# Optimization experiments

Hardware: AMD Instinct MI355X
Metric: run time of the kernel (lower is better)

## Reference

```python
import jax, jax.numpy as jnp
import numpy as np

B, LENGTH = 4, 65494
FILTS = 256        # sinc out channels == attention seq len == d_model (BN constraint)
KERNEL = 1025      # first_conv=1024 -> forced odd
D_MODEL = 256
N_HEADS = 8
D_FF = 1024
E_LAYERS = 4
C_OUT = 2
IN_SIZE = 21490
SR = 16000


def _to_mel(hz):
    return 2595 * np.log10(1 + hz / 700)


def _to_hz(mel):
    return 700 * (10 ** (mel / 2595) - 1)


def make_sinc_filters():
    out_ch = FILTS + 1
    f = (SR // 2) * np.linspace(0, 1, 257)  # NFFT=512 -> 257 bins
    fmel = _to_mel(f)
    mels = np.linspace(fmel.min(), fmel.max(), out_ch + 2)
    freq = _to_hz(mels)[:out_ch]
    hsupp = np.arange(-(KERNEL - 1) / 2, (KERNEL - 1) / 2 + 1)
    ham = np.hamming(KERNEL)
    bp = np.zeros((FILTS, KERNEL), dtype=np.float32)
    for i in range(FILTS):
        fmin, fmax = freq[i], freq[i + 1]
        h_hi = 2 * fmax / SR * np.sinc(2 * fmax * hsupp / SR)
        h_lo = 2 * fmin / SR * np.sinc(2 * fmin * hsupp / SR)
        bp[i] = (ham * (h_hi - h_lo)).astype(np.float32)
    return jnp.asarray(bp).reshape(FILTS, 1, KERNEL)


def layernorm(x, g, b, eps=1e-5):
    m = x.mean(-1, keepdims=True)
    v = x.var(-1, keepdims=True)
    return (x - m) / jnp.sqrt(v + eps) * g + b


def batchnorm(x, g, b, eps=1e-5):
    # training-mode BatchNorm1d over [B, C, T]: stats over (0, 2)
    m = x.mean((0, 2), keepdims=True)
    v = x.var((0, 2), keepdims=True)
    return (x - m) / jnp.sqrt(v + eps) * g[None, :, None] + b[None, :, None]


def positional(n):
    pos = jnp.arange(n, dtype=jnp.float32)[:, None]
    div = jnp.exp(jnp.arange(0, D_MODEL, 2, dtype=jnp.float32) * (-np.log(10000.0) / D_MODEL))
    pe = jnp.zeros((n, D_MODEL), jnp.float32)
    pe = pe.at[:, 0::2].set(jnp.sin(pos * div)).at[:, 1::2].set(jnp.cos(pos * div))
    return pe


def _forward(x, filters, bn1_g, bn1_b, emb_w, emb_b, embbn_g, embbn_b,
             wq, bq, wk, bk, wv, bv, wo, bo, c1w, c1b, c2w, c2b,
             ln1g, ln1b, ln2g, ln2b, lnfg, lnfb, projw, projb):
    Bb = x.shape[0]
    # SincConv: [B,1,L] -> [B, FILTS, L-K+1]
    h = jax.lax.conv_general_dilated(x[:, None, :], filters, (1,), 'VALID',
                                     dimension_numbers=('NCH', 'OIH', 'NCH'))
    h = jnp.abs(h)
    T = h.shape[-1] // 3
    h = h[..., :T * 3].reshape(Bb, FILTS, T, 3).max(-1)  # max_pool1d(k=3)
    h = jax.nn.selu(batchnorm(h, bn1_g, bn1_b))          # [B, FILTS, 21490]
    # LinearEmbedding: Linear(21490 -> d_model) + BN + ReLU + pos emb
    e = jnp.einsum('bct,dt->bcd', h, emb_w) + emb_b      # [B, FILTS, D_MODEL]
    e = jax.nn.relu(batchnorm(e, embbn_g, embbn_b))
    z = e + positional(e.shape[1])[None]
    hd = D_MODEL // N_HEADS
    scale = 1.0 / np.sqrt(hd)
    for l in range(E_LAYERS):
        q = (z @ wq[l].T + bq[l]).reshape(Bb, FILTS, N_HEADS, hd)
        k = (z @ wk[l].T + bk[l]).reshape(Bb, FILTS, N_HEADS, hd)
        v = (z @ wv[l].T + bv[l]).reshape(Bb, FILTS, N_HEADS, hd)
        scores = jnp.einsum('blhe,bshe->bhls', q, k) * scale  # mask_flag=False
        attn = jax.nn.softmax(scores, axis=-1)
        o = jnp.einsum('bhls,bshd->blhd', attn, v).reshape(Bb, FILTS, D_MODEL)
        o = o @ wo[l].T + bo[l]
        z = layernorm(z + o, ln1g[l], ln1b[l])
        y = jax.nn.gelu(jnp.einsum('bld,fd->blf', z, c1w[l]) + c1b[l], approximate=False)
        y = jnp.einsum('blf,df->bld', y, c2w[l]) + c2b[l]
        z = layernorm(z + y, ln2g[l], ln2b[l])
    z = layernorm(z, lnfg, lnfb)
    pooled = z.mean(axis=1)
    return pooled @ projw.T + projb  # [B, C_OUT]


def setup_inputs() -> dict:
    key = jax.random.key(0)
    ks = jax.random.split(key, 16)
    rn = lambda k, s, sc=0.02: jax.random.normal(k, s, jnp.float32) * sc
    d = {}
    d['x'] = jax.random.normal(ks[0], (B, LENGTH), jnp.float32)
    d['filters'] = make_sinc_filters()
    d['bn1_g'] = jnp.ones((FILTS,), jnp.float32)
    d['bn1_b'] = jnp.zeros((FILTS,), jnp.float32)
    d['emb_w'] = rn(ks[1], (D_MODEL, IN_SIZE))
    d['emb_b'] = jnp.zeros((D_MODEL,), jnp.float32)
    d['embbn_g'] = jnp.ones((D_MODEL,), jnp.float32)
    d['embbn_b'] = jnp.zeros((D_MODEL,), jnp.float32)
    d['wq'] = rn(ks[2], (E_LAYERS, D_MODEL, D_MODEL))
    d['bq'] = jnp.zeros((E_LAYERS, D_MODEL), jnp.float32)
    d['wk'] = rn(ks[3], (E_LAYERS, D_MODEL, D_MODEL))
    d['bk'] = jnp.zeros((E_LAYERS, D_MODEL), jnp.float32)
    d['wv'] = rn(ks[4], (E_LAYERS, D_MODEL, D_MODEL))
    d['bv'] = jnp.zeros((E_LAYERS, D_MODEL), jnp.float32)
    d['wo'] = rn(ks[5], (E_LAYERS, D_MODEL, D_MODEL))
    d['bo'] = jnp.zeros((E_LAYERS, D_MODEL), jnp.float32)
    d['c1w'] = rn(ks[6], (E_LAYERS, D_FF, D_MODEL))
    d['c1b'] = jnp.zeros((E_LAYERS, D_FF), jnp.float32)
    d['c2w'] = rn(ks[7], (E_LAYERS, D_MODEL, D_FF))
    d['c2b'] = jnp.zeros((E_LAYERS, D_MODEL), jnp.float32)
    d['ln1g'] = jnp.ones((E_LAYERS, D_MODEL), jnp.float32)
    d['ln1b'] = jnp.zeros((E_LAYERS, D_MODEL), jnp.float32)
    d['ln2g'] = jnp.ones((E_LAYERS, D_MODEL), jnp.float32)
    d['ln2b'] = jnp.zeros((E_LAYERS, D_MODEL), jnp.float32)
    d['lnfg'] = jnp.ones((D_MODEL,), jnp.float32)
    d['lnfb'] = jnp.zeros((D_MODEL,), jnp.float32)
    d['projw'] = rn(ks[8], (C_OUT, D_MODEL))
    d['projb'] = jnp.zeros((C_OUT,), jnp.float32)
    return d


def reference(x, filters, bn1_g, bn1_b, emb_w, emb_b, embbn_g, embbn_b,
              wq, bq, wk, bk, wv, bv, wo, bo, c1w, c1b, c2w, c2b,
              ln1g, ln1b, ln2g, ln2b, lnfg, lnfb, projw, projb):
    return _forward(x, filters, bn1_g, bn1_b, emb_w, emb_b, embbn_g, embbn_b,
                    wq, bq, wk, bk, wv, bv, wo, bo, c1w, c1b, c2w, c2b,
                    ln1g, ln1b, ln2g, ln2b, lnfg, lnfb, projw, projb)
```

## Files before the change

kernel.cpp:

```cpp
#include <hip/hip_runtime.h>
#include <math.h>

#define L_IN 65494
#define T_POOL 21490
#define TPP 21496
#define KF 1025
#define RS 1144
#define NCH 141
#define KEMB 21490
#define KEMBP 21504
#define NKC 1344
#define FTILE 33280
#define LWSZ 786432

typedef short s16x4 __attribute__((ext_vector_type(4)));
typedef _Float16 f16x8 __attribute__((ext_vector_type(8)));
typedef float f32x4 __attribute__((ext_vector_type(4)));
typedef float f32x16 __attribute__((ext_vector_type(16)));

__device__ inline float selu_f(float x) {
    float e = expf(fminf(x, 0.f));
    float neg = 1.6732632423543772f * (e - 1.f);
    return 1.0507009873554805f * (x > 0.f ? x : neg);
}

__device__ inline float gelu_f(float x) {
    return 0.5f * x * (1.f + erff(x * 0.7071067811865476f));
}

__device__ inline float dot4(float4 a, float4 b) {
    return fmaf(a.x, b.x, fmaf(a.y, b.y, fmaf(a.z, b.z, a.w * b.w)));
}

__device__ inline float sel4(float a0, float a1, float a2, float a3, int i) {
    float r = a0;
    r = (i == 1) ? a1 : r;
    r = (i == 2) ? a2 : r;
    r = (i == 3) ? a3 : r;
    return r;
}

__device__ inline short f2h_bits(float v) {
    _Float16 h = (_Float16)v;
    return *(short*)&h;
}

__device__ inline void f16split2(float v, _Float16& h, _Float16& l) {
    h = (_Float16)v;
    l = (_Float16)(v - (float)h);
}

__global__ __launch_bounds__(512)
void pack_all_kernel(const float* __restrict__ filt, const float* __restrict__ emb_w,
                     const float* __restrict__ wo, const float* __restrict__ wq,
                     const float* __restrict__ wk, const float* __restrict__ wv,
                     const float* __restrict__ c1w, const float* __restrict__ c2w,
                     short* __restrict__ fpH, short* __restrict__ wpH,
                     short* __restrict__ lw) {
    int bx = blockIdx.x;
    int t = threadIdx.x, lane = t >> 3, e = t & 7;
    if (bx < 520) {
        int ft = bx / 65, kc = bx % 65;
        int f = ft * 32 + (lane & 31);
        int tap = kc * 16 + (lane >> 5) * 8 + e;
        float v = (tap < KF) ? filt[f * KF + tap] : 0.f;
        fpH[bx * 512 + t] = f2h_bits(v);
    } else if (bx < 520 + 8 * NKC) {
        int blk = bx - 520;
        int ft = blk / NKC, kc = blk % NKC;
        int row = ft * 32 + (lane & 31);
        int tap = kc * 16 + (lane >> 5) * 8 + e;
        float v = (tap < KEMB) ? emb_w[(long)row * KEMB + tap] : 0.f;
        wpH[(long)blk * 512 + t] = f2h_bits(v);
    } else {
        int b = bx - 520 - 8 * NKC;
        int layer = b / 1536, r = b % 1536;
        const float* src;
        int K, t2;
        long dst;
        if (r < 512) {
            int mat = r >> 7; t2 = r & 127;
            const float* m0 = (mat == 0 ? wo : mat == 1 ? wq : mat == 2 ? wk : wv);
            src = m0 + (long)layer * 65536; K = 256;
            dst = (long)layer * LWSZ + (long)mat * 65536 + (long)t2 * 512;
        } else if (r < 1024) {
            t2 = r - 512;
            src = c1w + (long)layer * 262144; K = 256;
            dst = (long)layer * LWSZ + 262144 + (long)t2 * 512;
        } else {
            t2 = r - 1024;
            src = c2w + (long)layer * 262144; K = 1024;
            dst = (long)layer * LWSZ + 524288 + (long)t2 * 512;
        }
        int KB = K >> 5;
        int nt = t2 / KB, kb = t2 % KB;
        int n = nt * 16 + (lane & 15);
        int k = kb * 32 + ((lane >> 4) & 3) * 8 + e;
        lw[dst + t] = f2h_bits(src[(long)n * K + k]);
    }
}

__device__ inline f32x4 mfma_nt(const _Float16* __restrict__ Xh, const _Float16* __restrict__ Xl,
                                int xstride, const short* __restrict__ wp_nt, int KB, int lane) {
    f32x4 acc = {0.f, 0.f, 0.f, 0.f};
    const int row = (lane & 15) & 3;
    const int ko0 = ((lane >> 4) & 3) * 8;
    const short* bp = wp_nt + lane * 8;
    const _Float16* xh = Xh + row * xstride + ko0;
    const _Float16* xl = Xl + row * xstride + ko0;
#pragma unroll 8
    for (int kb = 0; kb < KB; kb++) {
        f16x8 bf = *(const f16x8*)(bp + kb * 512);
        f16x8 ah = *(const f16x8*)(xh + kb * 32);
        f16x8 al = *(const f16x8*)(xl + kb * 32);
        acc = __builtin_amdgcn_mfma_f32_16x16x32_f16(al, bf, acc, 0, 0, 0);
        acc = __builtin_amdgcn_mfma_f32_16x16x32_f16(ah, bf, acc, 0, 0, 0);
    }
    return acc;
}

union ConvLDS {
    short xh[8][RS];
    float ebuf[96][129];
};

__global__ __launch_bounds__(256, 3)
void conv_mfma_kernel(const float* __restrict__ x, const short* __restrict__ fpH,
                      _Float16* __restrict__ h) {
    __shared__ ConvLDS u;
    const int tid = threadIdx.x;
    const int pb = blockIdx.x;
    const int b = blockIdx.y;
    const int t0 = pb * 96;
    const float* xb = x + (long)b * L_IN;

    if (pb < 671) {
        for (int idx = tid; idx < 8 * NCH; idx += 256) {
            int s = idx / NCH, j = idx - s * NCH;
            int gi = t0 + s + j * 8;
            f16x8 hv;
#pragma unroll
            for (int e = 0; e < 8; e++) hv[e] = (_Float16)xb[gi + e];
            *(f16x8*)&u.xh[s][j * 8] = hv;
        }
    } else {
        for (int idx = tid; idx < 8 * NCH; idx += 256) {
            int s = idx / NCH, j = idx - s * NCH;
            int gi = t0 + s + j * 8;
            f16x8 hv;
#pragma unroll
            for (int e = 0; e < 8; e++) {
                float v = (gi + e < L_IN) ? xb[gi + e] : 0.f;
                hv[e] = (_Float16)v;
            }
            *(f16x8*)&u.xh[s][j * 8] = hv;
        }
    }
    __syncthreads();

    const int lane = tid & 63;
    const int wid = tid >> 6;
    const int l31 = lane & 31;
    const int hi = lane >> 5;
    const int f0w = wid * 64;

    const short* aH = &u.xh[l31 & 7][8 * (l31 >> 3) + 8 * hi];
    const short* bp0 = fpH + (long)(wid * 2) * FTILE + lane * 8;
    const short* bp1 = bp0 + FTILE;

    f32x16 a00 = {0}, a01 = {0}, a10 = {0}, a11 = {0}, a20 = {0}, a21 = {0};

#pragma unroll 1
    for (int kc = 0; kc < 65; kc++) {
        const int ko = kc * 16;
        const int kf = kc * 512;
        f16x8 ah0 = *(const f16x8*)(aH + ko);
        f16x8 ah1 = *(const f16x8*)(aH + ko + 32);
        f16x8 ah2 = *(const f16x8*)(aH + ko + 64);
        f16x8 bh0 = *(const f16x8*)(bp0 + kf);
        f16x8 bh1 = *(const f16x8*)(bp1 + kf);
        a00 = __builtin_amdgcn_mfma_f32_32x32x16_f16(ah0, bh0, a00, 0, 0, 0);
        a01 = __builtin_amdgcn_mfma_f32_32x32x16_f16(ah0, bh1, a01, 0, 0, 0);
        a10 = __builtin_amdgcn_mfma_f32_32x32x16_f16(ah1, bh0, a10, 0, 0, 0);
        a11 = __builtin_amdgcn_mfma_f32_32x32x16_f16(ah1, bh1, a11, 0, 0, 0);
        a20 = __builtin_amdgcn_mfma_f32_32x32x16_f16(ah2, bh0, a20, 0, 0, 0);
        a21 = __builtin_amdgcn_mfma_f32_32x32x16_f16(ah2, bh1, a21, 0, 0, 0);
    }

    __syncthreads();
    const int t3l = tid & 31;
    const int t3 = pb * 32 + t3l;

#pragma unroll
    for (int half = 0; half < 2; half++) {
        if ((wid >> 1) == half) {
            int fcb = f0w - half * 128;
#define WRF(ACC, MT, NT)                                                   \
            {                                                              \
                int fc = fcb + NT * 32 + l31;                              \
                _Pragma("unroll")                                          \
                for (int r = 0; r < 16; r++) {                             \
                    int pos = MT * 32 + (r & 3) + 8 * (r >> 2) + 4 * hi;   \
                    u.ebuf[pos][fc] = fabsf(ACC[r]);                       \
                }                                                          \
            }
            WRF(a00, 0, 0) WRF(a01, 0, 1)
            WRF(a10, 1, 0) WRF(a11, 1, 1)
            WRF(a20, 2, 0) WRF(a21, 2, 1)
#undef WRF
        }
        __syncthreads();
        if (t3 < T_POOL) {
            for (int ff = tid >> 5; ff < 128; ff += 8) {
                float v = fmaxf(fmaxf(u.ebuf[3 * t3l][ff], u.ebuf[3 * t3l + 1][ff]),
                                u.ebuf[3 * t3l + 2][ff]);
                h[((long)(b * 256 + half * 128 + ff)) * TPP + t3] = (_Float16)v;
            }
        }
        __syncthreads();
    }
}

__global__ __launch_bounds__(256)
void bn_part_kernel(const _Float16* __restrict__ xin, float* __restrict__ p1,
                    float* __restrict__ p2) {
    __shared__ float sm[8];
    int c = blockIdx.x, s = blockIdx.y, tid = threadIdx.x;
    int t0 = s * 2687, t1 = min(T_POOL, t0 + 2687);
    float s1 = 0.f, s2 = 0.f;
    for (int b = 0; b < 4; b++) {
        const _Float16* p = xin + (long)b * 256 * TPP + (long)c * TPP;
        for (int t = t0 + tid; t < t1; t += 256) {
            float v = (float)p[t];
            s1 += v;
            s2 = fmaf(v, v, s2);
        }
    }
    for (int off = 32; off > 0; off >>= 1) { s1 += __shfl_down(s1, off); s2 += __shfl_down(s2, off); }
    int lane = tid & 63, wv = tid >> 6;
    if (lane == 0) { sm[wv] = s1; sm[4 + wv] = s2; }
    __syncthreads();
    if (tid == 0) {
        p1[c * 8 + s] = sm[0] + sm[1] + sm[2] + sm[3];
        p2[c * 8 + s] = sm[4] + sm[5] + sm[6] + sm[7];
    }
}

__global__ __launch_bounds__(256)
void bn_fin_kernel(const float* __restrict__ p1, const float* __restrict__ p2,
                   const float* __restrict__ g, const float* __restrict__ bb,
                   float* __restrict__ sc, float* __restrict__ sh) {
    int c = threadIdx.x;
    float S1 = 0.f, S2 = 0.f;
#pragma unroll
    for (int s = 0; s < 8; s++) { S1 += p1[c * 8 + s]; S2 += p2[c * 8 + s]; }
    float n = 4.f * (float)T_POOL;
    float mean = S1 / n;
    float var = S2 / n - mean * mean;
    float rstd = rsqrtf(var + 1e-5f);
    float gc = g[c], bc = bb[c];
    sc[c] = rstd * gc;
    sh[c] = bc - mean * rstd * gc;
}

__global__ __launch_bounds__(256, 2)
void embed_mfma_kernel(const _Float16* __restrict__ H, const short* __restrict__ Wh,
                       const float* __restrict__ sc, const float* __restrict__ sh,
                       float* __restrict__ P, int kPerZ) {
    __shared__ short Ah[128][36];
    const int tid = threadIdx.x;
    const int rowBase = blockIdx.x * 128;
    const int colBase = blockIdx.y * 128;
    const int z = blockIdx.z;
    const int kz = z * kPerZ;
    const int iters = kPerZ >> 5;

    const int trow = tid >> 1, th = (tid & 1) * 16;
    const int arow = rowBase + trow;
    const float asc = sc[arow & 255], ash_ = sh[arow & 255];
    const _Float16* Ap = H + (long)arow * TPP;

    const int lane = tid & 63, wid = tid >> 6;
    const int l31 = lane & 31, hi = lane >> 5;
    const int wm = wid >> 1, wn = wid & 1;

    const short* bhp[2];
#pragma unroll
    for (int nt = 0; nt < 2; nt++) {
        int ft = (colBase >> 5) + wn * 2 + nt;
        bhp[nt] = Wh + (long)ft * NKC * 512 + lane * 8;
    }

    f32x16 acc[2][2] = {{{0}, {0}}, {{0}, {0}}};

    for (int it = 0; it < iters; it++) {
        const int k0 = kz + it * 32;
        __syncthreads();
        float av[16];
        if (k0 + 32 <= KEMB) {
            const f16x8* p8 = (const f16x8*)(Ap + k0 + th);
            f16x8 v0 = p8[0], v1 = p8[1];
#pragma unroll
            for (int e = 0; e < 8; e++) { av[e] = (float)v0[e]; av[8 + e] = (float)v1[e]; }
        } else {
#pragma unroll
            for (int e = 0; e < 16; e++) {
                int k = k0 + th + e;
                av[e] = (k < KEMB) ? (float)Ap[k] : 0.f;
            }
        }
#pragma unroll
        for (int q = 0; q < 4; q++) {
            s16x4 h4;
#pragma unroll
            for (int e = 0; e < 4; e++) {
                float v = selu_f(fmaf(av[q * 4 + e], asc, ash_));
                h4[e] = f2h_bits(v);
            }
            *(s16x4*)&Ah[trow][th + q * 4] = h4;
        }
        __syncthreads();

#pragma unroll
        for (int ks = 0; ks < 2; ks++) {
            const int kloc = ks * 16 + hi * 8;
            const long kcg = (long)((k0 >> 4) + ks) * 512;
            f16x8 ah[2], bh[2];
#pragma unroll
            for (int mt = 0; mt < 2; mt++) {
                const int r = wm * 64 + mt * 32 + l31;
                const short* ph = &Ah[r][kloc];
                union { f16x8 v; unsigned long long q[2]; } uh;
                uh.q[0] = *(const unsigned long long*)(ph);
                uh.q[1] = *(const unsigned long long*)(ph + 4);
                ah[mt] = uh.v;
            }
#pragma unroll
            for (int nt = 0; nt < 2; nt++)
                bh[nt] = *(const f16x8*)(bhp[nt] + kcg);
#pragma unroll
            for (int mt = 0; mt < 2; mt++)
#pragma unroll
                for (int nt = 0; nt < 2; nt++)
                    acc[mt][nt] = __builtin_amdgcn_mfma_f32_32x32x16_f16(ah[mt], bh[nt], acc[mt][nt], 0, 0, 0);
        }
    }

    float* Pz = P + (long)z * 262144;
#pragma unroll
    for (int mt = 0; mt < 2; mt++)
#pragma unroll
        for (int nt = 0; nt < 2; nt++) {
            int col = colBase + wn * 64 + nt * 32 + l31;
#pragma unroll
            for (int r = 0; r < 16; r++) {
                int row = rowBase + wm * 64 + mt * 32 + (r & 3) + 8 * (r >> 2) + 4 * hi;
                Pz[(long)row * 256 + col] = acc[mt][nt][r];
            }
        }
}

__global__ __launch_bounds__(256)
void embed_combine_kernel(const float* __restrict__ P, const float* __restrict__ eb,
                          float* __restrict__ e, float* __restrict__ ebnp, int nsplit) {
    __shared__ float sm[8];
    const int bid = blockIdx.x, tid = threadIdx.x;
    const int idx = bid * 256 + tid;
    float s = 0.f;
    for (int z = 0; z < nsplit; z++) s += P[(long)z * 262144 + idx];
    float v = s + eb[tid];
    e[idx] = v;
    float s1 = v, s2 = v * v;
    for (int off = 32; off > 0; off >>= 1) { s1 += __shfl_down(s1, off); s2 += __shfl_down(s2, off); }
    int lane = tid & 63, wv = tid >> 6;
    if (lane == 0) { sm[wv] = s1; sm[4 + wv] = s2; }
    __syncthreads();
    if (tid == 0) {
        ebnp[bid * 2] = sm[0] + sm[1] + sm[2] + sm[3];
        ebnp[bid * 2 + 1] = sm[4] + sm[5] + sm[6] + sm[7];
    }
}

__global__ __launch_bounds__(512)
void qkv_init_kernel(const float* __restrict__ e, const float* __restrict__ ebnp,
                     const float* __restrict__ bng, const float* __restrict__ bnb,
                     const short* __restrict__ lw0,
                     const float* __restrict__ bq0, const float* __restrict__ bk0,
                     const float* __restrict__ bv0,
                     float* __restrict__ z, float* __restrict__ qo,
                     float* __restrict__ ko, float* __restrict__ vo) {
    __shared__ _Float16 zsh[4][256], zsl[4][256];
    __shared__ float scs[4], shs[4];
    const int t = threadIdx.x;
    const int w = t >> 6, lane = t & 63;
    const long rowg0 = (long)blockIdx.x * 4;

    if (t < 4) {
        int c = (int)((rowg0 + t) & 255);
        float S1 = 0.f, S2 = 0.f;
#pragma unroll
        for (int b2 = 0; b2 < 4; b2++) {
            S1 += ebnp[(b2 * 256 + c) * 2];
            S2 += ebnp[(b2 * 256 + c) * 2 + 1];
        }
        float mean = S1 * (1.f / 1024.f);
        float var = S2 * (1.f / 1024.f) - mean * mean;
        float rstd = rsqrtf(var + 1e-5f);
        float gc = bng[c];
        scs[t] = rstd * gc;
        shs[t] = bnb[c] - mean * rstd * gc;
    }
    __syncthreads();

    for (int idx = t; idx < 1024; idx += 512) {
        int i = idx >> 8, dd = idx & 255;
        int c = (int)((rowg0 + i) & 255);
        float v = fmaf(e[(rowg0 + i) * 256 + dd], scs[i], shs[i]);
        v = fmaxf(v, 0.f);
        int i2 = dd >> 1;
        float ang = (float)c * expf(-0.03597789207803195f * (float)(2 * i2));
        float pe = (dd & 1) ? cosf(ang) : sinf(ang);
        float zz = v + pe;
        z[(rowg0 + i) * 256 + dd] = zz;
        _Float16 hh, ll;
        f16split2(zz, hh, ll);
        zsh[i][dd] = hh; zsl[i][dd] = ll;
    }
    __syncthreads();

#pragma unroll
    for (int mat = 0; mat < 3; mat++) {
        const short* wp = lw0 + 65536 * (1 + mat);
        const float* bb = (mat == 0 ? bq0 : mat == 1 ? bk0 : bv0);
        float* op = (mat == 0 ? qo : mat == 1 ? ko : vo);
        for (int nt = w; nt < 16; nt += 8) {
            f32x4 acc = mfma_nt(&zsh[0][0], &zsl[0][0], 256, wp + nt * 8 * 512, 8, lane);
            if (lane < 16) {
                int col = nt * 16 + lane;
                float bv2 = bb[col];
#pragma unroll
                for (int r = 0; r < 4; r++)
                    op[(rowg0 + r) * 256 + col] = acc[r] + bv2;
            }
        }
    }
}

__device__ inline void ln_reduce4(const float (*buf)[256], float (*mr)[2], int t) {
    int wid = t >> 6, lane = t & 63;
    if (wid < 4) {
        float4 v = *(const float4*)&buf[wid][lane * 4];
        float s = v.x + v.y + v.z + v.w;
        float q = v.x * v.x + v.y * v.y + v.z * v.z + v.w * v.w;
#pragma unroll
        for (int off = 32; off > 0; off >>= 1) {
            s += __shfl_xor(s, off);
            q += __shfl_xor(q, off);
        }
        if (lane == 0) {
            float mean = s * (1.f / 256.f);
            float var = q * (1.f / 256.f) - mean * mean;
            mr[wid][0] = mean;
            mr[wid][1] = rsqrtf(var + 1e-5f);
        }
    }
}

template <int LAST>
__global__ __launch_bounds__(1024)
void layer_kernel(const float* __restrict__ zin, const float* __restrict__ qin,
                  const float* __restrict__ kin, const float* __restrict__ vin,
                  const short* __restrict__ lw_l, const short* __restrict__ lw_n,
                  const float* __restrict__ bo_l,
                  const float* __restrict__ c1b_l, const float* __restrict__ c2b_l,
                  const float* __restrict__ ln1g_l, const float* __restrict__ ln1b_l,
                  const float* __restrict__ ln2g_l, const float* __restrict__ ln2b_l,
                  const float* __restrict__ bq_n, const float* __restrict__ bk_n,
                  const float* __restrict__ bv_n,
                  const float* __restrict__ lnfg, const float* __restrict__ lnfb,
                  float* __restrict__ zout, float* __restrict__ qo,
                  float* __restrict__ ko, float* __restrict__ vo,
                  float* __restrict__ lnf_out) {
    __shared__ float zs[4][256];
    __shared__ float qb[4][256];
    __shared__ float sscore[4][8][256];
    __shared__ _Float16 zsh[4][256], zsl[4][256];
    __shared__ _Float16 yh[4][1024], yl[4][1024];
    __shared__ float mr[4][2];

    const int t = threadIdx.x;
    const int w = t >> 6, lane = t & 63;
    const long rowg0 = (long)blockIdx.x * 4;
    const int b = blockIdx.x >> 6;

    const int f = t & 255;
    const int kq = t >> 8;

    {
        int r = t >> 8, dd = t & 255;
        zs[r][dd] = zin[(rowg0 + r) * 256 + dd];
        qb[r][dd] = qin[(rowg0 + r) * 256 + dd];
    }
    __syncthreads();

    {
        const float scale = 0.17677669529663687f;
        const int jq = lane >> 3, li = lane & 7, d4 = li * 4;
        const int hh = w >> 1, jh = w & 1;
        const float* kb = kin + (long)b * 65536 + hh * 32 + d4;
        float4 q0 = *(const float4*)&qb[0][hh * 32 + d4];
        float4 q1 = *(const float4*)&qb[1][hh * 32 + d4];
        float4 q2 = *(const float4*)&qb[2][hh * 32 + d4];
        float4 q3 = *(const float4*)&qb[3][hh * 32 + d4];
        for (int jb = 0; jb < 16; jb++) {
            int j = jh * 128 + jb * 8 + jq;
            float4 kv = *(const float4*)(kb + (long)j * 256);
            float a0 = dot4(kv, q0), a1 = dot4(kv, q1);
            float a2 = dot4(kv, q2), a3 = dot4(kv, q3);
#pragma unroll
            for (int off = 1; off < 8; off <<= 1) {
                a0 += __shfl_xor(a0, off); a1 += __shfl_xor(a1, off);
                a2 += __shfl_xor(a2, off); a3 += __shfl_xor(a3, off);
            }
            if (li < 4) sscore[li][hh][j] = sel4(a0, a1, a2, a3, li) * scale;
        }
    }
    __syncthreads();

    {
#pragma unroll
        for (int p = 0; p < 2; p++) {
            int pair = w * 2 + p;
            int i = pair >> 3, hh = pair & 7;
            float* row = sscore[i][hh];
            float v0 = row[lane], v1 = row[lane + 64];
            float v2 = row[lane + 128], v3 = row[lane + 192];
            float m = fmaxf(fmaxf(v0, v1), fmaxf(v2, v3));
#pragma unroll
            for (int off = 32; off > 0; off >>= 1) m = fmaxf(m, __shfl_xor(m, off));
            float e0 = expf(v0 - m), e1 = expf(v1 - m);
            float e2 = expf(v2 - m), e3 = expf(v3 - m);
            float su = e0 + e1 + e2 + e3;
#pragma unroll
            for (int off = 32; off > 0; off >>= 1) su += __shfl_xor(su, off);
            float inv = 1.f / su;
            row[lane] = e0 * inv; row[lane + 64] = e1 * inv;
            row[lane + 128] = e2 * inv; row[lane + 192] = e3 * inv;
        }
    }
    __syncthreads();

    {
        int row = kq;
        int hh = f >> 5;
        const float* vcol = vin + (long)b * 65536 + f;
        const float* p0 = sscore[row][hh];
        float a0 = 0.f;
#pragma unroll 8
        for (int j4 = 0; j4 < 64; j4++) {
            float4 pv0 = *(const float4*)(p0 + j4 * 4);
            float v0 = vcol[(long)(j4 * 4 + 0) * 256];
            float v1 = vcol[(long)(j4 * 4 + 1) * 256];
            float v2 = vcol[(long)(j4 * 4 + 2) * 256];
            float v3 = vcol[(long)(j4 * 4 + 3) * 256];
            a0 = fmaf(pv0.x, v0, a0); a0 = fmaf(pv0.y, v1, a0);
            a0 = fmaf(pv0.z, v2, a0); a0 = fmaf(pv0.w, v3, a0);
        }
        _Float16 hh2, ll;
        f16split2(a0, hh2, ll);
        zsh[row][f] = hh2; zsl[row][f] = ll;
    }
    __syncthreads();

    {
        int nt = w;
        f32x4 acc = mfma_nt(&zsh[0][0], &zsl[0][0], 256, lw_l + nt * 8 * 512, 8, lane);
        if (lane < 16) {
            int col = nt * 16 + lane;
            float bb = bo_l[col];
#pragma unroll
            for (int r = 0; r < 4; r++)
                qb[r][col] = acc[r] + bb + zs[r][col];
        }
    }
    __syncthreads();
    ln_reduce4(qb, mr, t);
    __syncthreads();
    {
        int r = kq;
        float z1 = (qb[r][f] - mr[r][0]) * mr[r][1] * ln1g_l[f] + ln1b_l[f];
        zs[r][f] = z1;
        _Float16 hh2, ll;
        f16split2(z1, hh2, ll);
        zsh[r][f] = hh2; zsl[r][f] = ll;
    }
    __syncthreads();

    {
        const short* wp = lw_l + 262144;
        for (int nt = w; nt < 64; nt += 16) {
            f32x4 acc = mfma_nt(&zsh[0][0], &zsl[0][0], 256, wp + nt * 8 * 512, 8, lane);
            if (lane < 16) {
                int col = nt * 16 + lane;
                float cb = c1b_l[col];
#pragma unroll
                for (int r = 0; r < 4; r++) {
                    float g = gelu_f(acc[r] + cb);
                    _Float16 hh2, ll;
                    f16split2(g, hh2, ll);
                    yh[r][col] = hh2; yl[r][col] = ll;
                }
            }
        }
    }
    __syncthreads();

    {
        const short* wp = lw_l + 524288;
        int nt = w;
        f32x4 acc = mfma_nt(&yh[0][0], &yl[0][0], 1024, wp + nt * 32 * 512, 32, lane);
        if (lane < 16) {
            int col = nt * 16 + lane;
            float cb = c2b_l[col];
#pragma unroll
            for (int r = 0; r < 4; r++)
                qb[r][col] = acc[r] + cb + zs[r][col];
        }
    }
    __syncthreads();
    ln_reduce4(qb, mr, t);
    __syncthreads();
    {
        int r = kq;
        float z2 = (qb[r][f] - mr[r][0]) * mr[r][1] * ln2g_l[f] + ln2b_l[f];
        zs[r][f] = z2;
        zout[(rowg0 + r) * 256 + f] = z2;
        _Float16 hh2, ll;
        f16split2(z2, hh2, ll);
        zsh[r][f] = hh2; zsl[r][f] = ll;
    }
    __syncthreads();

    if (!LAST) {
#pragma unroll
        for (int mat = 0; mat < 3; mat++) {
            const short* wp = lw_n + 65536 * (1 + mat);
            const float* bb = (mat == 0 ? bq_n : mat == 1 ? bk_n : bv_n);
            float* op = (mat == 0 ? qo : mat == 1 ? ko : vo);
            int nt = w;
            f32x4 acc = mfma_nt(&zsh[0][0], &zsl[0][0], 256, wp + nt * 8 * 512, 8, lane);
            if (lane < 16) {
                int col = nt * 16 + lane;
                float bv2 = bb[col];
#pragma unroll
                for (int r = 0; r < 4; r++)
                    op[(rowg0 + r) * 256 + col] = acc[r] + bv2;
            }
        }
    } else {
        ln_reduce4(zs, mr, t);
        __syncthreads();
        {
            int r = kq;
            lnf_out[(rowg0 + r) * 256 + f] =
                (zs[r][f] - mr[r][0]) * mr[r][1] * lnfg[f] + lnfb[f];
        }
    }
}

__global__ __launch_bounds__(256)
void final_kernel(const float* __restrict__ zf, const float* __restrict__ pw,
                  const float* __restrict__ pb, float* __restrict__ out) {
    __shared__ float sm[8];
    int b = blockIdx.x, d = threadIdx.x;
    float s = 0.f;
    for (int c = 0; c < 256; c++) s += zf[((long)(b * 256 + c)) * 256 + d];
    float pooled = s * (1.f / 256.f);
    float c0 = pooled * pw[d], c1 = pooled * pw[256 + d];
    for (int off = 32; off > 0; off >>= 1) { c0 += __shfl_down(c0, off); c1 += __shfl_down(c1, off); }
    int lane = d & 63, wv = d >> 6;
    if (lane == 0) { sm[wv] = c0; sm[4 + wv] = c1; }
    __syncthreads();
    if (d == 0) {
        out[b * 2 + 0] = sm[0] + sm[1] + sm[2] + sm[3] + pb[0];
        out[b * 2 + 1] = sm[4] + sm[5] + sm[6] + sm[7] + pb[1];
    }
}

extern "C" void kernel_launch(void* const* d_in, const int* in_sizes, int n_in,
                              void* d_out, int out_size, void* d_ws, size_t ws_size,
                              hipStream_t stream) {
    const float* x       = (const float*)d_in[0];
    const float* filters = (const float*)d_in[1];
    const float* bn1_g   = (const float*)d_in[2];
    const float* bn1_b   = (const float*)d_in[3];
    const float* emb_w   = (const float*)d_in[4];
    const float* emb_b   = (const float*)d_in[5];
    const float* embbn_g = (const float*)d_in[6];
    const float* embbn_b = (const float*)d_in[7];
    const float* wq      = (const float*)d_in[8];
    const float* bq      = (const float*)d_in[9];
    const float* wk      = (const float*)d_in[10];
    const float* bk      = (const float*)d_in[11];
    const float* wv      = (const float*)d_in[12];
    const float* bv      = (const float*)d_in[13];
    const float* wo      = (const float*)d_in[14];
    const float* bo      = (const float*)d_in[15];
    const float* c1w     = (const float*)d_in[16];
    const float* c1b     = (const float*)d_in[17];
    const float* c2w     = (const float*)d_in[18];
    const float* c2b     = (const float*)d_in[19];
    const float* ln1g    = (const float*)d_in[20];
    const float* ln1b    = (const float*)d_in[21];
    const float* ln2g    = (const float*)d_in[22];
    const float* ln2b    = (const float*)d_in[23];
    const float* lnfg    = (const float*)d_in[24];
    const float* lnfb    = (const float*)d_in[25];
    const float* projw   = (const float*)d_in[26];
    const float* projb   = (const float*)d_in[27];

    const long hF = 11005952L;
    const long wpackF = 2752512L;
    const long lwF = 1572864L;
    const long fixedF = hF + 6656 + wpackF + lwF + 9L * 262144;
    long wsFloats = (long)(ws_size / 4);
    long Z = 32;
    while (Z > 8 && fixedF + Z * 262144L > wsFloats) Z >>= 1;
    const int kPerZ = KEMBP / (int)Z;

    float* ws = (float*)d_ws;
    _Float16* h16 = (_Float16*)ws;
    float* bn1_sc = ws + hF;
    float* bn1_sh = bn1_sc + 256;
    float* ebnp   = bn1_sh + 256;
    float* bnp1   = ebnp + 2048;
    float* bnp2   = bnp1 + 2048;
    float* part   = bnp2 + 2048;
    float* wsp    = part + Z * 262144L;
    short* wpH    = (short*)wsp;
    float* e      = wsp + wpackF;
    float* z      = e + 262144;
    float* qA     = z + 262144;
    float* kA     = qA + 262144;
    float* vA     = kA + 262144;
    float* qB     = vA + 262144;
    float* kB     = qB + 262144;
    float* vB     = kB + 262144;
    float* t1     = vB + 262144;
    short* lw     = (short*)(t1 + 262144);

    short* fpH = (short*)part;

    pack_all_kernel<<<520 + 8 * NKC + 6144, 512, 0, stream>>>(
        filters, emb_w, wo, wq, wk, wv, c1w, c2w, fpH, wpH, lw);
    conv_mfma_kernel<<<dim3(672, 4), 256, 0, stream>>>(x, fpH, h16);
    bn_part_kernel<<<dim3(256, 8), 256, 0, stream>>>(h16, bnp1, bnp2);
    bn_fin_kernel<<<1, 256, 0, stream>>>(bnp1, bnp2, bn1_g, bn1_b, bn1_sc, bn1_sh);
    embed_mfma_kernel<<<dim3(8, 2, (int)Z), 256, 0, stream>>>(h16, wpH,
                                                              bn1_sc, bn1_sh, part, kPerZ);
    embed_combine_kernel<<<1024, 256, 0, stream>>>(part, emb_b, e, ebnp, (int)Z);
    qkv_init_kernel<<<256, 512, 0, stream>>>(e, ebnp, embbn_g, embbn_b, lw,
                                             bq, bk, bv, z, qA, kA, vA);

    float* qs[2][3] = {{qA, kA, vA}, {qB, kB, vB}};
    for (int l = 0; l < 4; l++) {
        float** in = qs[l & 1];
        float** ou = qs[(l + 1) & 1];
        const short* lw_l = lw + (long)l * LWSZ;
        const short* lw_n = lw + (long)((l + 1) & 3) * LWSZ;
        const float* bo_l = bo + l * 256;
        const float* c1b_l = c1b + l * 1024;
        const float* c2b_l = c2b + l * 256;
        const float* l1g = ln1g + l * 256; const float* l1b = ln1b + l * 256;
        const float* l2g = ln2g + l * 256; const float* l2b = ln2b + l * 256;
        if (l < 3) {
            const float* bq_n = bq + (l + 1) * 256;
            const float* bk_n = bk + (l + 1) * 256;
            const float* bv_n = bv + (l + 1) * 256;
            layer_kernel<0><<<256, 1024, 0, stream>>>(z, in[0], in[1], in[2],
                lw_l, lw_n, bo_l, c1b_l, c2b_l, l1g, l1b, l2g, l2b,
                bq_n, bk_n, bv_n, lnfg, lnfb,
                z, ou[0], ou[1], ou[2], t1);
        } else {
            layer_kernel<1><<<256, 1024, 0, stream>>>(z, in[0], in[1], in[2],
                lw_l, lw_n, bo_l, c1b_l, c2b_l, l1g, l1b, l2g, l2b,
                bq, bk, bv, lnfg, lnfb,
                z, ou[0], ou[1], ou[2], t1);
        }
    }

    final_kernel<<<4, 256, 0, stream>>>(t1, projw, projb, (float*)d_out);
}
```

Measured before the change: 450.9 us.

## Split encoder layer blocks to two rows each with 512 threads

Each layer_kernel block now handles 2 sequence rows instead of 4, giving 512 blocks of 512 threads rather than 256 of 1024, so more of the GPU's CUs get work. The MFMA tiles still span 4 rows, so the unused rows 2-3 of the fp16 staging buffers are zeroed and the extra N-tiles are covered by looping each wave. The cost is that weights and K/V are re-read by twice as many blocks, and half of every MFMA's rows are wasted padding.

```diff
diff --git a/kernel.cpp b/kernel.cpp
--- a/kernel.cpp
+++ b/kernel.cpp
@@ -446,9 +446,9 @@
     }
 }
 
-__device__ inline void ln_reduce4(const float (*buf)[256], float (*mr)[2], int t) {
+__device__ inline void ln_reduce2(const float (*buf)[256], float (*mr)[2], int t) {
     int wid = t >> 6, lane = t & 63;
-    if (wid < 4) {
+    if (wid < 2) {
         float4 v = *(const float4*)&buf[wid][lane * 4];
         float s = v.x + v.y + v.z + v.w;
         float q = v.x * v.x + v.y * v.y + v.z * v.z + v.w * v.w;
@@ -467,7 +467,7 @@
 }
 
 template <int LAST>
-__global__ __launch_bounds__(1024)
+__global__ __launch_bounds__(512)
 void layer_kernel(const float* __restrict__ zin, const float* __restrict__ qin,
                   const float* __restrict__ kin, const float* __restrict__ vin,
                   const short* __restrict__ lw_l, const short* __restrict__ lw_n,
@@ -481,48 +481,48 @@
                   float* __restrict__ zout, float* __restrict__ qo,
                   float* __restrict__ ko, float* __restrict__ vo,
                   float* __restrict__ lnf_out) {
-    __shared__ float zs[4][256];
-    __shared__ float qb[4][256];
-    __shared__ float sscore[4][8][256];
+    __shared__ float zs[2][256];
+    __shared__ float qb[2][256];
+    __shared__ float sscore[2][8][256];
     __shared__ _Float16 zsh[4][256], zsl[4][256];
     __shared__ _Float16 yh[4][1024], yl[4][1024];
-    __shared__ float mr[4][2];
+    __shared__ float mr[2][2];
 
     const int t = threadIdx.x;
     const int w = t >> 6, lane = t & 63;
-    const long rowg0 = (long)blockIdx.x * 4;
-    const int b = blockIdx.x >> 6;
+    const long rowg0 = (long)blockIdx.x * 2;
+    const int b = blockIdx.x >> 7;
 
     const int f = t & 255;
-    const int kq = t >> 8;
-
-    {
-        int r = t >> 8, dd = t & 255;
-        zs[r][dd] = zin[(rowg0 + r) * 256 + dd];
-        qb[r][dd] = qin[(rowg0 + r) * 256 + dd];
+    const int rp = t >> 8;
+
+    {
+        zs[rp][f] = zin[(rowg0 + rp) * 256 + f];
+        qb[rp][f] = qin[(rowg0 + rp) * 256 + f];
+        f16x8 zv = {0, 0, 0, 0, 0, 0, 0, 0};
+        if (t < 64) *(f16x8*)&zsh[2][t * 8] = zv;
+        else if (t < 128) *(f16x8*)&zsl[2][(t - 64) * 8] = zv;
+        if (t < 256) *(f16x8*)&yh[2][t * 8] = zv;
+        else *(f16x8*)&yl[2][(t - 256) * 8] = zv;
     }
     __syncthreads();
 
     {
         const float scale = 0.17677669529663687f;
         const int jq = lane >> 3, li = lane & 7, d4 = li * 4;
-        const int hh = w >> 1, jh = w & 1;
-        const float* kb = kin + (long)b * 65536 + hh * 32 + d4;
-        float4 q0 = *(const float4*)&qb[0][hh * 32 + d4];
-        float4 q1 = *(const float4*)&qb[1][hh * 32 + d4];
-        float4 q2 = *(const float4*)&qb[2][hh * 32 + d4];
-        float4 q3 = *(const float4*)&qb[3][hh * 32 + d4];
-        for (int jb = 0; jb < 16; jb++) {
-            int j = jh * 128 + jb * 8 + jq;
+        const float* kb = kin + (long)b * 65536 + w * 32 + d4;
+        float4 q0 = *(const float4*)&qb[0][w * 32 + d4];
+        float4 q1 = *(const float4*)&qb[1][w * 32 + d4];
+        for (int jb = 0; jb < 32; jb++) {
+            int j = jb * 8 + jq;
             float4 kv = *(const float4*)(kb + (long)j * 256);
             float a0 = dot4(kv, q0), a1 = dot4(kv, q1);
-            float a2 = dot4(kv, q2), a3 = dot4(kv, q3);
 #pragma unroll
             for (int off = 1; off < 8; off <<= 1) {
-                a0 += __shfl_xor(a0, off); a1 += __shfl_xor(a1, off);
-                a2 += __shfl_xor(a2, off); a3 += __shfl_xor(a3, off);
-            }
-            if (li < 4) sscore[li][hh][j] = sel4(a0, a1, a2, a3, li) * scale;
+                a0 += __shfl_xor(a0, off);
+                a1 += __shfl_xor(a1, off);
+            }
+            if (li < 2) sscore[li][w][j] = (li == 0 ? a0 : a1) * scale;
         }
     }
     __syncthreads();
@@ -551,10 +551,9 @@
     __syncthreads();
 
     {
-        int row = kq;
         int hh = f >> 5;
         const float* vcol = vin + (long)b * 65536 + f;
-        const float* p0 = sscore[row][hh];
+        const float* p0 = sscore[rp][hh];
         float a0 = 0.f;
 #pragma unroll 8
         for (int j4 = 0; j4 < 64; j4++) {
@@ -568,43 +567,43 @@
         }
         _Float16 hh2, ll;
         f16split2(a0, hh2, ll);
-        zsh[row][f] = hh2; zsl[row][f] = ll;
-    }
-    __syncthreads();
-
-    {
-        int nt = w;
-        f32x4 acc = mfma_nt(&zsh[0][0], &zsl[0][0], 256, lw_l + nt * 8 * 512, 8, lane);
-        if (lane < 16) {
-            int col = nt * 16 + lane;
-            float bb = bo_l[col];
-#pragma unroll
-            for (int r = 0; r < 4; r++)
-                qb[r][col] = acc[r] + bb + zs[r][col];
-        }
-    }
-    __syncthreads();
-    ln_reduce4(qb, mr, t);
-    __syncthreads();
-    {
-        int r = kq;
-        float z1 = (qb[r][f] - mr[r][0]) * mr[r][1] * ln1g_l[f] + ln1b_l[f];
-        zs[r][f] = z1;
+        zsh[rp][f] = hh2; zsl[rp][f] = ll;
+    }
+    __syncthreads();
+
+    {
+        for (int nt = w; nt < 16; nt += 8) {
+            f32x4 acc = mfma_nt(&zsh[0][0], &zsl[0][0], 256, lw_l + nt * 8 * 512, 8, lane);
+            if (lane < 16) {
+                int col = nt * 16 + lane;
+                float bb2 = bo_l[col];
+#pragma unroll
+                for (int r = 0; r < 2; r++)
+                    qb[r][col] = acc[r] + bb2 + zs[r][col];
+            }
+        }
+    }
+    __syncthreads();
+    ln_reduce2(qb, mr, t);
+    __syncthreads();
+    {
+        float z1 = (qb[rp][f] - mr[rp][0]) * mr[rp][1] * ln1g_l[f] + ln1b_l[f];
+        zs[rp][f] = z1;
         _Float16 hh2, ll;
         f16split2(z1, hh2, ll);
-        zsh[r][f] = hh2; zsl[r][f] = ll;
+        zsh[rp][f] = hh2; zsl[rp][f] = ll;
     }
     __syncthreads();
 
     {
         const short* wp = lw_l + 262144;
-        for (int nt = w; nt < 64; nt += 16) {
+        for (int nt = w; nt < 64; nt += 8) {
             f32x4 acc = mfma_nt(&zsh[0][0], &zsl[0][0], 256, wp + nt * 8 * 512, 8, lane);
             if (lane < 16) {
                 int col = nt * 16 + lane;
                 float cb = c1b_l[col];
 #pragma unroll
-                for (int r = 0; r < 4; r++) {
+                for (int r = 0; r < 2; r++) {
                     float g = gelu_f(acc[r] + cb);
                     _Float16 hh2, ll;
                     f16split2(g, hh2, ll);
@@ -617,27 +616,27 @@
 
     {
         const short* wp = lw_l + 524288;
-        int nt = w;
-        f32x4 acc = mfma_nt(&yh[0][0], &yl[0][0], 1024, wp + nt * 32 * 512, 32, lane);
-        if (lane < 16) {
-            int col = nt * 16 + lane;
-            float cb = c2b_l[col];
-#pragma unroll
-            for (int r = 0; r < 4; r++)
-                qb[r][col] = acc[r] + cb + zs[r][col];
-        }
-    }
-    __syncthreads();
-    ln_reduce4(qb, mr, t);
-    __syncthreads();
-    {
-        int r = kq;
-        float z2 = (qb[r][f] - mr[r][0]) * mr[r][1] * ln2g_l[f] + ln2b_l[f];
-        zs[r][f] = z2;
-        zout[(rowg0 + r) * 256 + f] = z2;
+        for (int nt = w; nt < 16; nt += 8) {
+            f32x4 acc = mfma_nt(&yh[0][0], &yl[0][0], 1024, wp + nt * 32 * 512, 32, lane);
+            if (lane < 16) {
+                int col = nt * 16 + lane;
+                float cb = c2b_l[col];
+#pragma unroll
+                for (int r = 0; r < 2; r++)
+                    qb[r][col] = acc[r] + cb + zs[r][col];
+            }
+        }
+    }
+    __syncthreads();
+    ln_reduce2(qb, mr, t);
+    __syncthreads();
+    {
+        float z2 = (qb[rp][f] - mr[rp][0]) * mr[rp][1] * ln2g_l[f] + ln2b_l[f];
+        zs[rp][f] = z2;
+        zout[(rowg0 + rp) * 256 + f] = z2;
         _Float16 hh2, ll;
         f16split2(z2, hh2, ll);
-        zsh[r][f] = hh2; zsl[r][f] = ll;
+        zsh[rp][f] = hh2; zsl[rp][f] = ll;
     }
     __syncthreads();
 
@@ -645,25 +644,25 @@
 #pragma unroll
         for (int mat = 0; mat < 3; mat++) {
             const short* wp = lw_n + 65536 * (1 + mat);
-            const float* bb = (mat == 0 ? bq_n : mat == 1 ? bk_n : bv_n);
+            const float* bb2 = (mat == 0 ? bq_n : mat == 1 ? bk_n : bv_n);
             float* op = (mat == 0 ? qo : mat == 1 ? ko : vo);
-            int nt = w;
-            f32x4 acc = mfma_nt(&zsh[0][0], &zsl[0][0], 256, wp + nt * 8 * 512, 8, lane);
-            if (lane < 16) {
-                int col = nt * 16 + lane;
-                float bv2 = bb[col];
-#pragma unroll
-                for (int r = 0; r < 4; r++)
-                    op[(rowg0 + r) * 256 + col] = acc[r] + bv2;
+            for (int nt = w; nt < 16; nt += 8) {
+                f32x4 acc = mfma_nt(&zsh[0][0], &zsl[0][0], 256, wp + nt * 8 * 512, 8, lane);
+                if (lane < 16) {
+                    int col = nt * 16 + lane;
+                    float bv2 = bb2[col];
+#pragma unroll
+                    for (int r = 0; r < 2; r++)
+                        op[(rowg0 + r) * 256 + col] = acc[r] + bv2;
+                }
             }
         }
     } else {
-        ln_reduce4(zs, mr, t);
+        ln_reduce2(zs, mr, t);
         __syncthreads();
         {
-            int r = kq;
-            lnf_out[(rowg0 + r) * 256 + f] =
-                (zs[r][f] - mr[r][0]) * mr[r][1] * lnfg[f] + lnfb[f];
+            lnf_out[(rowg0 + rp) * 256 + f] =
+                (zs[rp][f] - mr[rp][0]) * mr[rp][1] * lnfg[f] + lnfb[f];
         }
     }
 }
@@ -777,12 +776,12 @@
             const float* bq_n = bq + (l + 1) * 256;
             const float* bk_n = bk + (l + 1) * 256;
             const float* bv_n = bv + (l + 1) * 256;
-            layer_kernel<0><<<256, 1024, 0, stream>>>(z, in[0], in[1], in[2],
+            layer_kernel<0><<<512, 512, 0, stream>>>(z, in[0], in[1], in[2],
                 lw_l, lw_n, bo_l, c1b_l, c2b_l, l1g, l1b, l2g, l2b,
                 bq_n, bk_n, bv_n, lnfg, lnfb,
                 z, ou[0], ou[1], ou[2], t1);
         } else {
-            layer_kernel<1><<<256, 1024, 0, stream>>>(z, in[0], in[1], in[2],
+            layer_kernel<1><<<512, 512, 0, stream>>>(z, in[0], in[1], in[2],
                 lw_l, lw_n, bo_l, c1b_l, c2b_l, l1g, l1b, l2g, l2b,
                 bq, bk, bv, lnfg, lnfb,
                 z, ou[0], ou[1], ou[2], t1);
```

New measurement: 523.7 us. +16.1%, slower.
